# Kernel tuning notes

Measured on AMD Instinct MI355X. Metric: run time of the kernel, lower is better.

## Reference

```python
import jax, jax.numpy as jnp
import numpy as np

NUM_EMB = 256
EMB_DIM = 128
COMMIT_COST = 0.25


def setup_inputs() -> dict:
    key = jax.random.key(0)
    k1, k2 = jax.random.split(key)
    z = jax.random.normal(k1, (64, EMB_DIM, 64, 64), dtype=jnp.float32)
    # codebook initialized uniform(-1/num_embeddings, 1/num_embeddings)
    emb = jax.random.uniform(k2, (NUM_EMB, EMB_DIM), dtype=jnp.float32,
                             minval=-1.0 / NUM_EMB, maxval=1.0 / NUM_EMB)
    return {"z": z, "emb": emb}


def reference(z, emb):
    B, C, H, W = z.shape
    # [B, C, H, W] -> [B*H*W, C]
    z_flat = jnp.transpose(z, (0, 2, 3, 1)).reshape(-1, C)
    # squared L2 distances to each code: ||z||^2 - 2 z.e + ||e||^2, shape [N, K]
    d = (jnp.sum(z_flat * z_flat, axis=1, keepdims=True)
         - 2.0 * jnp.einsum('nc,kc->nk', z_flat, emb)
         + jnp.sum(emb * emb, axis=1))
    idx = jnp.argmin(d, axis=1)  # [N]
    # gather codes, back to NCHW
    quantized = emb[idx].reshape(B, H, W, C)
    quantized = jnp.transpose(quantized, (0, 3, 1, 2))
    commitment_loss = COMMIT_COST * jnp.mean(
        (jax.lax.stop_gradient(quantized) - z) ** 2)
    codebook_loss = jnp.mean((quantized - jax.lax.stop_gradient(z)) ** 2)
    # straight-through estimator
    quantized_ste = z + jax.lax.stop_gradient(quantized - z)
    return (quantized_ste, idx.reshape(B, H, W), commitment_loss, codebook_loss)
```

## Files before the change

### kernel.cpp

```cpp
#include <hip/hip_runtime.h>

#define K_EMB   256
#define C_DIM   128
#define HW      4096
#define NPOS    262144
#define Q_ELEMS 33554432
#define IDX_OFF Q_ELEMS
#define LOSS_OFF (Q_ELEMS + NPOS)

#define TK 64

#define WS_ENORM 0
#define WS_ACC   256
#define WS_EMBT  512
#define WS_NEED_FULL  ((WS_EMBT + C_DIM * K_EMB) * 4)

__global__ __launch_bounds__(K_EMB) void vq_prep(const float* __restrict__ emb,
                                                 float* __restrict__ ws,
                                                 int use_embT) {
    int k = threadIdx.x;
    float s = 0.f;
    #pragma unroll 8
    for (int c = 0; c < C_DIM; ++c) {
        float e = emb[k * C_DIM + c];
        s = fmaf(e, e, s);
        if (use_embT) ws[WS_EMBT + c * K_EMB + k] = e;
    }
    ws[WS_ENORM + k] = s;
    if (k == 0) ws[WS_ACC] = 0.f;
}

template <int UT, int ZN>
__device__ __forceinline__ void vq_chunk(const float* __restrict__ zp,
                                         const float* __restrict__ embT,
                                         const float* __restrict__ emb,
                                         int kc, float* __restrict__ acc,
                                         float& znorm) {
    #pragma unroll
    for (int j = 0; j < TK; ++j) acc[j] = 0.f;

    #pragma unroll 2
    for (int c = 0; c < C_DIM; ++c) {
        float zc = zp[(size_t)c * HW];
        if (ZN) znorm = fmaf(zc, zc, znorm);
        if (UT) {
            const float* __restrict__ ep = embT + c * K_EMB + kc;
            #pragma unroll
            for (int j = 0; j < TK; ++j)
                acc[j] = fmaf(zc, ep[j], acc[j]);
        } else {
            #pragma unroll
            for (int j = 0; j < TK; ++j)
                acc[j] = fmaf(zc, emb[(kc + j) * C_DIM + c], acc[j]);
        }
    }
}

template <int UT>
__global__ __launch_bounds__(256, 4) void vq_main(const float* __restrict__ z,
                                                  const float* __restrict__ emb,
                                                  const float* __restrict__ ws,
                                                  float* __restrict__ out,
                                                  float* __restrict__ loss_acc) {
    const int pos = blockIdx.x * 256 + threadIdx.x;
    const int b   = pos >> 12;
    const int hw  = pos & 4095;

    const float* __restrict__ zp    = z + (size_t)b * (C_DIM * HW) + hw;
    const float* __restrict__ embT  = ws + WS_EMBT;
    const float* __restrict__ enorm = ws + WS_ENORM;

    float znorm = 0.f;
    float best  = 3.402823466e38f;
    int   bidx  = 0;
    float acc[TK];

    vq_chunk<UT, 1>(zp, embT, emb, 0, acc, znorm);
    #pragma unroll
    for (int j = 0; j < TK; ++j) {
        float d = (znorm - 2.0f * acc[j]) + enorm[j];
        if (d < best) { best = d; bidx = j; }
    }

    for (int kc = TK; kc < K_EMB; kc += TK) {
        vq_chunk<UT, 0>(zp, embT, emb, kc, acc, znorm);
        #pragma unroll
        for (int j = 0; j < TK; ++j) {
            float d = (znorm - 2.0f * acc[j]) + enorm[kc + j];
            if (d < best) { best = d; bidx = kc + j; }
        }
    }

    __builtin_nontemporal_store((float)bidx, &out[IDX_OFF + pos]);

    float lsum = 0.f;
    float* qp = out + (size_t)b * (C_DIM * HW) + hw;
    #pragma unroll 4
    for (int c = 0; c < C_DIM; ++c) {
        float zc = zp[(size_t)c * HW];
        float e  = UT ? embT[c * K_EMB + bidx] : emb[bidx * C_DIM + c];
        float dq = e - zc;
        lsum = fmaf(dq, dq, lsum);
        __builtin_nontemporal_store(zc + dq, &qp[(size_t)c * HW]);
    }

    #pragma unroll
    for (int off = 32; off > 0; off >>= 1)
        lsum += __shfl_down(lsum, off, 64);
    if ((threadIdx.x & 63) == 0) atomicAdd(loss_acc, lsum);
}

__global__ void vq_finalize(const float* __restrict__ loss_acc,
                            float* __restrict__ out_losses) {
    float S = loss_acc[0];
    float mean = S / (float)Q_ELEMS;
    out_losses[0] = 0.25f * mean;
    out_losses[1] = mean;
}

extern "C" void kernel_launch(void* const* d_in, const int* in_sizes, int n_in,
                              void* d_out, int out_size, void* d_ws, size_t ws_size,
                              hipStream_t stream) {
    const float* z   = (const float*)d_in[0];
    const float* emb = (const float*)d_in[1];
    float* out = (float*)d_out;
    float* ws  = (float*)d_ws;

    int use_embT = (ws_size >= (size_t)WS_NEED_FULL) ? 1 : 0;

    vq_prep<<<1, K_EMB, 0, stream>>>(emb, ws, use_embT);
    if (use_embT)
        vq_main<1><<<NPOS / 256, 256, 0, stream>>>(z, emb, ws, out, ws + WS_ACC);
    else
        vq_main<0><<<NPOS / 256, 256, 0, stream>>>(z, emb, ws, out, ws + WS_ACC);
    vq_finalize<<<1, 1, 0, stream>>>(ws + WS_ACC, out + LOSS_OFF);
}
```

Before: 459.7 us.

## Split codebook search across two thread halves per position with shared-memory argmin merge

Each block now handles 128 positions with 256 threads, and each half of the block scans half of the 256 codes. Partial argmins are merged through shared memory, after which only the first half writes the quantized output and loss. The chunk size drops from 64 to 32 and launch bounds rise to 6 waves per SIMD, cutting registers to raise occupancy. The cost is that z is read twice per position, half the threads sit idle during the write phase, and a block barrier is added; on ties between halves the lower index is kept, matching argmin.

Result: slower. 1.336 ms (+190.6%).

```diff
diff --git a/kernel.cpp b/kernel.cpp
--- a/kernel.cpp
+++ b/kernel.cpp
@@ -8,7 +8,8 @@
 #define IDX_OFF Q_ELEMS
 #define LOSS_OFF (Q_ELEMS + NPOS)
 
-#define TK 64
+#define TK 32
+#define KHALF 128
 
 #define WS_ENORM 0
 #define WS_ACC   256
@@ -57,14 +58,17 @@
 }
 
 template <int UT>
-__global__ __launch_bounds__(256, 4) void vq_main(const float* __restrict__ z,
+__global__ __launch_bounds__(256, 6) void vq_main(const float* __restrict__ z,
                                                   const float* __restrict__ emb,
                                                   const float* __restrict__ ws,
                                                   float* __restrict__ out,
                                                   float* __restrict__ loss_acc) {
-    const int pos = blockIdx.x * 256 + threadIdx.x;
-    const int b   = pos >> 12;
-    const int hw  = pos & 4095;
+    const int t    = threadIdx.x;
+    const int p    = t & (KHALF - 1);
+    const int half = t >> 7;
+    const int pos  = blockIdx.x * KHALF + p;
+    const int b    = pos >> 12;
+    const int hw   = pos & 4095;
 
     const float* __restrict__ zp    = z + (size_t)b * (C_DIM * HW) + hw;
     const float* __restrict__ embT  = ws + WS_EMBT;
@@ -75,14 +79,16 @@
     int   bidx  = 0;
     float acc[TK];
 
-    vq_chunk<UT, 1>(zp, embT, emb, 0, acc, znorm);
+    const int kbase = half * KHALF;
+
+    vq_chunk<UT, 1>(zp, embT, emb, kbase, acc, znorm);
     #pragma unroll
     for (int j = 0; j < TK; ++j) {
-        float d = (znorm - 2.0f * acc[j]) + enorm[j];
-        if (d < best) { best = d; bidx = j; }
+        float d = (znorm - 2.0f * acc[j]) + enorm[kbase + j];
+        if (d < best) { best = d; bidx = kbase + j; }
     }
 
-    for (int kc = TK; kc < K_EMB; kc += TK) {
+    for (int kc = kbase + TK; kc < kbase + KHALF; kc += TK) {
         vq_chunk<UT, 0>(zp, embT, emb, kc, acc, znorm);
         #pragma unroll
         for (int j = 0; j < TK; ++j) {
@@ -91,23 +97,37 @@
         }
     }
 
-    __builtin_nontemporal_store((float)bidx, &out[IDX_OFF + pos]);
+    __shared__ float sh_best[256];
+    __shared__ int   sh_bidx[256];
+    sh_best[t] = best;
+    sh_bidx[t] = bidx;
+    __syncthreads();
 
-    float lsum = 0.f;
-    float* qp = out + (size_t)b * (C_DIM * HW) + hw;
-    #pragma unroll 4
-    for (int c = 0; c < C_DIM; ++c) {
-        float zc = zp[(size_t)c * HW];
-        float e  = UT ? embT[c * K_EMB + bidx] : emb[bidx * C_DIM + c];
-        float dq = e - zc;
-        lsum = fmaf(dq, dq, lsum);
-        __builtin_nontemporal_store(zc + dq, &qp[(size_t)c * HW]);
+    const float blo = sh_best[p];
+    const int   ilo = sh_bidx[p];
+    const float bhi = sh_best[KHALF + p];
+    const int   ihi = sh_bidx[KHALF + p];
+    const int   fin = (bhi < blo) ? ihi : ilo;
+
+    if (half == 0) {
+        __builtin_nontemporal_store((float)fin, &out[IDX_OFF + pos]);
+
+        float lsum = 0.f;
+        float* qp = out + (size_t)b * (C_DIM * HW) + hw;
+        #pragma unroll 4
+        for (int c = 0; c < C_DIM; ++c) {
+            float zc = zp[(size_t)c * HW];
+            float e  = UT ? embT[c * K_EMB + fin] : emb[fin * C_DIM + c];
+            float dq = e - zc;
+            lsum = fmaf(dq, dq, lsum);
+            __builtin_nontemporal_store(zc + dq, &qp[(size_t)c * HW]);
+        }
+
+        #pragma unroll
+        for (int off = 32; off > 0; off >>= 1)
+            lsum += __shfl_down(lsum, off, 64);
+        if ((t & 63) == 0) atomicAdd(loss_acc, lsum);
     }
-
-    #pragma unroll
-    for (int off = 32; off > 0; off >>= 1)
-        lsum += __shfl_down(lsum, off, 64);
-    if ((threadIdx.x & 63) == 0) atomicAdd(loss_acc, lsum);
 }
 
 __global__ void vq_finalize(const float* __restrict__ loss_acc,
@@ -130,8 +150,8 @@
 
     vq_prep<<<1, K_EMB, 0, stream>>>(emb, ws, use_embT);
     if (use_embT)
-        vq_main<1><<<NPOS / 256, 256, 0, stream>>>(z, emb, ws, out, ws + WS_ACC);
+        vq_main<1><<<NPOS / KHALF, 256, 0, stream>>>(z, emb, ws, out, ws + WS_ACC);
     else
-        vq_main<0><<<NPOS / 256, 256, 0, stream>>>(z, emb, ws, out, ws + WS_ACC);
+        vq_main<0><<<NPOS / KHALF, 256, 0, stream>>>(z, emb, ws, out, ws + WS_ACC);
     vq_finalize<<<1, 1, 0, stream>>>(ws + WS_ACC, out + LOSS_OFF);
 }
```
